# Kernel optimization log

Hardware: AMD Instinct MI355X
Metric: run time of the kernel (lower is better)

The kernel has to match this reference:

```python
import jax, jax.numpy as jnp
import numpy as np

NUM_JOINTS = 32
N_E = 1024
E_DIM = 128
BETA = 0.25
HID = 256
CHAINS = [[0,1,2,3,4,5],[0,6,7,8,9,10],[0,11,12,13,14,15],
          [12,16,17,18,19,20,21,22,23],[12,24,25,26,27,28,29,30,31]]


def setup_inputs() -> dict:
    key = jax.random.key(0)
    ks = jax.random.split(key, 8)
    B, T = 64, 128
    z = jax.random.normal(ks[0], (B, T, NUM_JOINTS, E_DIM), jnp.float32)
    # xavier_uniform for embeddings: bound = sqrt(6/(n_e+e_dim))
    eb = float(np.sqrt(6.0 / (N_E + E_DIM)))
    emb = jax.random.uniform(ks[1], (NUM_JOINTS, N_E, E_DIM), jnp.float32, -eb, eb)
    # torch Linear default init: U(-1/sqrt(fan_in), 1/sqrt(fan_in))
    b1b = float(1.0 / np.sqrt(2 * E_DIM))
    W1 = jax.random.uniform(ks[2], (2 * E_DIM, HID), jnp.float32, -b1b, b1b)
    b1 = jax.random.uniform(ks[3], (HID,), jnp.float32, -b1b, b1b)
    ln_g = jnp.ones((HID,), jnp.float32)
    ln_b = jnp.zeros((HID,), jnp.float32)
    b2b = float(1.0 / np.sqrt(HID))
    W2 = jax.random.uniform(ks[4], (HID, E_DIM), jnp.float32, -b2b, b2b)
    b2 = jax.random.uniform(ks[5], (E_DIM,), jnp.float32, -b2b, b2b)
    return {"z": z, "emb": emb, "W1": W1, "b1": b1, "ln_g": ln_g,
            "ln_b": ln_b, "W2": W2, "b2": b2}


def _layernorm(x, g, b, eps=1e-5):
    m = jnp.mean(x, axis=-1, keepdims=True)
    v = jnp.mean((x - m) ** 2, axis=-1, keepdims=True)
    return (x - m) * jax.lax.rsqrt(v + eps) * g + b


def _mlp(x, W1, b1, ln_g, ln_b, W2, b2):
    h = x @ W1 + b1
    h = jax.nn.relu(_layernorm(h, ln_g, ln_b))
    return h @ W2 + b2


def _quantize_joint(h, E):
    # h: [B,T,C], E: [n_e,C]. argmin of euclidean dist == argmin of -2 h.E^T + |E|^2
    B, T, C = h.shape
    hf = h.reshape(-1, C)
    d = -2.0 * (hf @ E.T) + jnp.sum(E * E, axis=1)  # [B*T, n_e]
    idx = jnp.argmin(d, axis=1)
    e = E[idx].reshape(B, T, C)  # one-hot @ E == gather
    sg = jax.lax.stop_gradient
    loss = jnp.mean((sg(e) - h) ** 2) + BETA * jnp.mean((e - sg(h)) ** 2)
    q = h + sg(e - h)  # straight-through
    return q, e, idx.reshape(B, T), loss


def reference(z, emb, W1, b1, ln_g, ln_b, W2, b2):
    B, T, V, C = z.shape
    sg = jax.lax.stop_gradient
    stored_q, stored_e, stored_idx = {}, {}, {}
    total = jnp.zeros((), z.dtype)
    for chain in CHAINS:
        parent_e = None
        for i, j in enumerate(chain):
            if j not in stored_q:  # single-pass per joint
                zj = z[:, :, j, :]
                h = _mlp(jnp.concatenate([parent_e, zj], -1), W1, b1, ln_g, ln_b, W2, b2) if i > 0 else zj
                q, e, idx, loss = _quantize_joint(h, emb[j])
                stored_q[j], stored_e[j], stored_idx[j] = q, e, idx
                total = total + loss
            parent_e = sg(stored_e[j])
    z_q = jnp.stack([stored_q[v] for v in range(V)], axis=2)      # [B,T,V,C]
    indices = jnp.stack([stored_idx[v] for v in range(V)], axis=2)  # [B,T,V]
    return z_q, total / V, indices
```

## Files before the change

kernel.cpp:

```cpp
#include <hip/hip_runtime.h>

#define NJ 32
#define NE 1024
#define CD 128
#define HID 256
#define ROWS 8192

struct Lv { int nj; int j[5]; int p[5]; };

__global__ __launch_bounds__(256) void norms_kernel(const float* __restrict__ emb,
                                                    float* __restrict__ nrm) {
  int gid = blockIdx.x * 256 + threadIdx.x;
  int n = gid >> 2, l = gid & 3;
  const float* row = emb + (size_t)n * CD;
  float s = 0.f;
#pragma unroll
  for (int i = 0; i < 8; ++i) {
    float4 v = *(const float4*)&row[(l + 4 * i) * 4];
    s += v.x * v.x + v.y * v.y + v.z * v.z + v.w * v.w;
  }
  s += __shfl_xor(s, 1);
  s += __shfl_xor(s, 2);
  if (l == 0) nrm[n] = s;
}

template <int RB>
__global__ __launch_bounds__(256) void fused_level(
    const float* __restrict__ z, const float* __restrict__ emb,
    const float* __restrict__ W1, const float* __restrict__ b1,
    const float* __restrict__ lng, const float* __restrict__ lnb,
    const float* __restrict__ W2, const float* __restrict__ b2,
    const float* __restrict__ nrm,
    float* __restrict__ zq, float* __restrict__ idx_out,
    float* __restrict__ partials, Lv lv, int pbase) {
  constexpr int RPG = RB / 8;
  constexpr int R4 = RB / 4;
  constexpr int HSP = RB + 4;
  constexpr int BPJ = ROWS / RB;
  constexpr int XS_SZ = 32 * HSP;
  constexpr int HS_SZ = 128 * HSP;
  constexpr int P1 = XS_SZ + 8448;
  constexpr int P3 = HS_SZ + 2112;
  constexpr int P4 = HS_SZ + 16 * 516 + 512;
  constexpr int SM12 = (P1 > P3) ? P1 : P3;
  constexpr int SMEM = (SM12 > P4) ? SM12 : P4;

  __shared__ __align__(16) float smem[SMEM];
  __shared__ float wsum[4];
  float* xs  = smem;
  float* ws1 = smem + XS_SZ;
  float* as_ = smem;
  float* ws2 = smem + HS_SZ;
  float* hs  = smem;
  float* es  = smem + HS_SZ;
  float* nsm = smem + HS_SZ + 16 * 516;

  const int tid = threadIdx.x;
  const int rg = tid >> 5, cg = tid & 31;
  const int u = cg & 15;
  const int qcA = (cg >> 4) * 128 + u * 4;
  const int qcB = qcA + 64;
  const int jl = blockIdx.x / BPJ;
  const int row0 = (blockIdx.x % BPJ) * RB;
  const int jj = lv.j[jl], pj = lv.p[jl];
  const size_t rstride = (size_t)NJ * CD;

  if (pj >= 0) {
    float acc1[RPG][8];
#pragma unroll
    for (int r = 0; r < RPG; ++r)
#pragma unroll
      for (int c = 0; c < 8; ++c) acc1[r][c] = 0.f;

#pragma unroll 1
    for (int ks = 0; ks < 8; ++ks) {
#pragma unroll
      for (int uu = 0; uu < RB / 32; ++uu) {
        int idx = uu * 256 + tid;
        int r = idx >> 3, kq = idx & 7;
        const float* src = (ks < 4)
            ? (zq + (size_t)(row0 + r) * rstride + (size_t)pj * CD + (ks * 32 + kq * 4))
            : (z  + (size_t)(row0 + r) * rstride + (size_t)jj * CD + (ks * 32 - 128 + kq * 4));
        float4 v = *(const float4*)src;
        xs[(kq * 4 + 0) * HSP + r] = v.x;
        xs[(kq * 4 + 1) * HSP + r] = v.y;
        xs[(kq * 4 + 2) * HSP + r] = v.z;
        xs[(kq * 4 + 3) * HSP + r] = v.w;
      }
#pragma unroll
      for (int v8 = 0; v8 < 8; ++v8) {
        int idx = v8 * 256 + tid;
        int k = idx >> 6, c4 = idx & 63;
        *(float4*)&ws1[k * 264 + c4 * 4] =
            *(const float4*)&W1[(size_t)(ks * 32 + k) * HID + c4 * 4];
      }
      __syncthreads();
#pragma unroll 2
      for (int kk = 0; kk < 32; ++kk) {
        float xr[RPG], wc[8];
#pragma unroll
        for (int g = 0; g < RPG / 4; ++g)
          *(float4*)&xr[g * 4] = *(const float4*)&xs[kk * HSP + rg * RPG + g * 4];
        *(float4*)&wc[0] = *(const float4*)&ws1[kk * 264 + qcA];
        *(float4*)&wc[4] = *(const float4*)&ws1[kk * 264 + qcB];
#pragma unroll
        for (int r = 0; r < RPG; ++r)
#pragma unroll
          for (int c = 0; c < 8; ++c)
            acc1[r][c] += xr[r] * wc[c];
      }
      __syncthreads();
    }

    {
      float bb[8], gg[8], be[8];
      *(float4*)&bb[0] = *(const float4*)&b1[qcA];
      *(float4*)&bb[4] = *(const float4*)&b1[qcB];
      *(float4*)&gg[0] = *(const float4*)&lng[qcA];
      *(float4*)&gg[4] = *(const float4*)&lng[qcB];
      *(float4*)&be[0] = *(const float4*)&lnb[qcA];
      *(float4*)&be[4] = *(const float4*)&lnb[qcB];
#pragma unroll
      for (int r = 0; r < RPG; ++r) {
        float s0 = 0.f, q0 = 0.f;
#pragma unroll
        for (int j = 0; j < 8; ++j) {
          float v = acc1[r][j] + bb[j];
          acc1[r][j] = v;
          s0 += v; q0 += v * v;
        }
        float si = __shfl_xor(s0, 16), qi = __shfl_xor(q0, 16);
        float s1 = si, q1 = qi;
#pragma unroll
        for (int j = 0; j < 8; ++j) {
          float v = acc1[r][j];
          s1 += v; q1 += v * v;
        }
#pragma unroll
        for (int m = 1; m < 16; m <<= 1) {
          s1 += __shfl_xor(s1, m); q1 += __shfl_xor(q1, m);
        }
        float s2 = __shfl_xor(s1, 16), q2 = __shfl_xor(q1, 16);
        float Sx = (cg & 16) ? s1 : s2;
        float Qx = (cg & 16) ? q1 : q2;
        float mu = Sx * (1.f / HID);
        float va = Qx * (1.f / HID) - mu * mu;
        float iv = 1.f / sqrtf(va + 1e-5f);
#pragma unroll
        for (int j = 0; j < 8; ++j) {
          float a = (acc1[r][j] - mu) * iv * gg[j] + be[j];
          acc1[r][j] = fmaxf(a, 0.f);
        }
      }
    }

    float acc2[RPG][4];
#pragma unroll
    for (int r = 0; r < RPG; ++r)
#pragma unroll
      for (int c = 0; c < 4; ++c) acc2[r][c] = 0.f;

#pragma unroll 1
    for (int half = 0; half < 2; ++half) {
      __syncthreads();
      if ((cg >> 4) == half) {
#pragma unroll
        for (int j = 0; j < 8; ++j) {
          int kl = (j >> 2) * 64 + u * 4 + (j & 3);
#pragma unroll
          for (int g = 0; g < RPG / 4; ++g)
            *(float4*)&as_[kl * HSP + rg * RPG + g * 4] =
                make_float4(acc1[g * 4 + 0][j], acc1[g * 4 + 1][j],
                            acc1[g * 4 + 2][j], acc1[g * 4 + 3][j]);
        }
      }
      __syncthreads();
#pragma unroll 1
      for (int kc = 0; kc < 8; ++kc) {
#pragma unroll
        for (int v = 0; v < 2; ++v) {
          int idx = v * 256 + tid;
          int k = idx >> 5, c4 = idx & 31;
          *(float4*)&ws2[k * 132 + c4 * 4] =
              *(const float4*)&W2[(size_t)(half * 128 + kc * 16 + k) * CD + c4 * 4];
        }
        __syncthreads();
#pragma unroll 2
        for (int kk = 0; kk < 16; ++kk) {
          float ar[RPG], wc2[4];
#pragma unroll
          for (int g = 0; g < RPG / 4; ++g)
            *(float4*)&ar[g * 4] =
                *(const float4*)&as_[(kc * 16 + kk) * HSP + rg * RPG + g * 4];
          *(float4*)&wc2[0] = *(const float4*)&ws2[kk * 132 + cg * 4];
#pragma unroll
          for (int r = 0; r < RPG; ++r)
#pragma unroll
            for (int c = 0; c < 4; ++c)
              acc2[r][c] += ar[r] * wc2[c];
        }
        __syncthreads();
      }
    }
    {
      float4 bv = *(const float4*)&b2[cg * 4];
      float bb2[4] = {bv.x, bv.y, bv.z, bv.w};
#pragma unroll
      for (int c = 0; c < 4; ++c) {
#pragma unroll
        for (int g = 0; g < RPG / 4; ++g)
          *(float4*)&hs[(cg * 4 + c) * HSP + rg * RPG + g * 4] =
              make_float4(acc2[g * 4 + 0][c] + bb2[c], acc2[g * 4 + 1][c] + bb2[c],
                          acc2[g * 4 + 2][c] + bb2[c], acc2[g * 4 + 3][c] + bb2[c]);
      }
    }
  } else {
#pragma unroll
    for (int v = 0; v < RB / 8; ++v) {
      int idx = v * 256 + tid;
      int r = idx >> 5, c4 = idx & 31;
      float4 vz = *(const float4*)&z[(size_t)(row0 + r) * rstride + (size_t)jj * CD + c4 * 4];
      hs[(c4 * 4 + 0) * HSP + r] = vz.x;
      hs[(c4 * 4 + 1) * HSP + r] = vz.y;
      hs[(c4 * 4 + 2) * HSP + r] = vz.z;
      hs[(c4 * 4 + 3) * HSP + r] = vz.w;
    }
  }

  const int w4 = tid >> 6;
  const int l4 = tid & 63;
  float mnv[R4]; int mni[R4];
#pragma unroll
  for (int r = 0; r < R4; ++r) { mnv[r] = 3.402823e38f; mni[r] = 0; }
  const float* embJ = emb + (size_t)jj * NE * CD;
  const float* nrmJ = nrm + jj * NE;

#pragma unroll 1
  for (int p = 0; p < 2; ++p) {
    __syncthreads();
    if (tid < 128) {
      *(float4*)&nsm[tid * 4] = *(const float4*)&nrmJ[p * 512 + tid * 4];
    }
    float acc4[R4][8];
#pragma unroll
    for (int r = 0; r < R4; ++r)
#pragma unroll
      for (int c = 0; c < 8; ++c) acc4[r][c] = 0.f;

#pragma unroll 1
    for (int kc = 0; kc < 8; ++kc) {
#pragma unroll
      for (int v = 0; v < 8; ++v) {
        int idx = v * 256 + tid;
        int n = idx >> 2, kq = idx & 3;
        float4 ev = *(const float4*)&embJ[(size_t)(p * 512 + n) * CD + kc * 16 + kq * 4];
        es[(kq * 4 + 0) * 516 + n] = ev.x;
        es[(kq * 4 + 1) * 516 + n] = ev.y;
        es[(kq * 4 + 2) * 516 + n] = ev.z;
        es[(kq * 4 + 3) * 516 + n] = ev.w;
      }
      __syncthreads();
#pragma unroll 2
      for (int kk = 0; kk < 16; ++kk) {
        int c = kc * 16 + kk;
        float hr[R4], ec[8];
#pragma unroll
        for (int g = 0; g < R4 / 4; ++g)
          *(float4*)&hr[g * 4] = *(const float4*)&hs[c * HSP + w4 * R4 + g * 4];
        *(float4*)&ec[0] = *(const float4*)&es[kk * 516 + l4 * 4];
        *(float4*)&ec[4] = *(const float4*)&es[kk * 516 + 256 + l4 * 4];
#pragma unroll
        for (int r = 0; r < R4; ++r)
#pragma unroll
          for (int c2 = 0; c2 < 8; ++c2)
            acc4[r][c2] += hr[r] * ec[c2];
      }
      __syncthreads();
    }
#pragma unroll
    for (int r = 0; r < R4; ++r) {
#pragma unroll
      for (int q = 0; q < 2; ++q) {
#pragma unroll
        for (int j = 0; j < 4; ++j) {
          int nl = q * 256 + l4 * 4 + j;
          float d = nsm[nl] - 2.f * acc4[r][q * 4 + j];
          int n = p * 512 + nl;
          if (d < mnv[r]) { mnv[r] = d; mni[r] = n; }
        }
      }
    }
  }

#pragma unroll
  for (int r = 0; r < R4; ++r) {
    float mv = mnv[r]; int mi = mni[r];
#pragma unroll
    for (int m = 1; m < 64; m <<= 1) {
      float om = __shfl_xor(mv, m); int oi = __shfl_xor(mi, m);
      if (om < mv || (om == mv && oi < mi)) { mv = om; mi = oi; }
    }
    mnv[r] = mv; mni[r] = mi;
  }

  float lsum = 0.f;
#pragma unroll
  for (int r = 0; r < R4; ++r) {
    int row = w4 * R4 + r;
    int id = mni[r];
    const float* erow = embJ + (size_t)id * CD;
    float2 ev = *(const float2*)&erow[l4 * 2];
    float h0 = hs[(l4 * 2 + 0) * HSP + row];
    float h1 = hs[(l4 * 2 + 1) * HSP + row];
    float dx = ev.x - h0, dy = ev.y - h1;
    lsum += dx * dx + dy * dy;
    *(float2*)&zq[(size_t)(row0 + row) * rstride + (size_t)jj * CD + l4 * 2] = ev;
    if (l4 == r) idx_out[(size_t)(row0 + row) * NJ + jj] = (float)id;
  }
#pragma unroll
  for (int m = 1; m < 64; m <<= 1) lsum += __shfl_xor(lsum, m);
  if (l4 == 0) wsum[w4] = lsum;
  __syncthreads();
  if (tid == 0) partials[pbase + blockIdx.x] = wsum[0] + wsum[1] + wsum[2] + wsum[3];
}

__global__ __launch_bounds__(256) void loss_reduce(const float* __restrict__ p, int n,
                                                   float* __restrict__ out) {
  __shared__ float ws[4];
  float s = 0.f;
  for (int i = threadIdx.x; i < n; i += 256) s += p[i];
#pragma unroll
  for (int m = 1; m < 64; m <<= 1) s += __shfl_xor(s, m);
  if ((threadIdx.x & 63) == 0) ws[threadIdx.x >> 6] = s;
  __syncthreads();
  if (threadIdx.x == 0)
    out[0] = (ws[0] + ws[1] + ws[2] + ws[3]) * (1.25f / (1048576.f * 32.f));
}

extern "C" void kernel_launch(void* const* d_in, const int* in_sizes, int n_in,
                              void* d_out, int out_size, void* d_ws, size_t ws_size,
                              hipStream_t stream) {
  const float* z = (const float*)d_in[0];
  const float* emb = (const float*)d_in[1];
  const float* W1 = (const float*)d_in[2];
  const float* b1 = (const float*)d_in[3];
  const float* lng = (const float*)d_in[4];
  const float* lnb = (const float*)d_in[5];
  const float* W2 = (const float*)d_in[6];
  const float* b2 = (const float*)d_in[7];

  float* zq = (float*)d_out;
  float* loss = zq + (size_t)ROWS * NJ * CD;
  float* idxo = loss + 1;

  float* nrm = (float*)d_ws;
  float* partials = nrm + NJ * NE;

  norms_kernel<<<NJ * NE * 4 / 256, 256, 0, stream>>>(emb, nrm);

  static const Lv levels[11] = {
      {1, {0, 0, 0, 0, 0}, {-1, 0, 0, 0, 0}},
      {3, {1, 6, 11, 0, 0}, {0, 0, 0, 0, 0}},
      {3, {2, 7, 12, 0, 0}, {1, 6, 11, 0, 0}},
      {5, {3, 8, 13, 16, 24}, {2, 7, 12, 12, 12}},
      {5, {4, 9, 14, 17, 25}, {3, 8, 13, 16, 24}},
      {5, {5, 10, 15, 18, 26}, {4, 9, 14, 17, 25}},
      {2, {19, 27, 0, 0, 0}, {18, 26, 0, 0, 0}},
      {2, {20, 28, 0, 0, 0}, {19, 27, 0, 0, 0}},
      {2, {21, 29, 0, 0, 0}, {20, 28, 0, 0, 0}},
      {2, {22, 30, 0, 0, 0}, {21, 29, 0, 0, 0}},
      {2, {23, 31, 0, 0, 0}, {22, 30, 0, 0, 0}},
  };
  static const int rbs[11] = {16, 64, 64, 64, 64, 64, 32, 32, 32, 32, 32};

  int pbase = 0;
  for (int L = 0; L < 11; ++L) {
    int bpj = ROWS / rbs[L];
    int blocks = levels[L].nj * bpj;
    if (rbs[L] == 64) {
      fused_level<64><<<blocks, 256, 0, stream>>>(
          z, emb, W1, b1, lng, lnb, W2, b2, nrm, zq, idxo, partials, levels[L], pbase);
    } else if (rbs[L] == 32) {
      fused_level<32><<<blocks, 256, 0, stream>>>(
          z, emb, W1, b1, lng, lnb, W2, b2, nrm, zq, idxo, partials, levels[L], pbase);
    } else {
      fused_level<16><<<blocks, 256, 0, stream>>>(
          z, emb, W1, b1, lng, lnb, W2, b2, nrm, zq, idxo, partials, levels[L], pbase);
    }
    pbase += blocks;
  }
  loss_reduce<<<1, 256, 0, stream>>>(partials, pbase, loss);
}
```

Measured before the change: 1.877 ms.

## Stage full MLP input once and read weights directly from global memory

The first MLP matmul now loads the whole 256-wide input tile into shared memory in one pass and runs a single K loop, reading W1 straight from global/L1 instead of staging 32-row chunks with per-chunk barriers. The second matmul is retiled to 16x16 threads with 8 output columns each, again reading W2 from global memory and removing its staged chunk loop. This is meant to cut barrier and shared-memory staging overhead. The cost is a larger input shared buffer, which may lower occupancy, and weight reads that now depend on cache hits.

Result: slower. 1.955 ms (+4.2%).

```diff
diff --git a/kernel.cpp b/kernel.cpp
--- a/kernel.cpp
+++ b/kernel.cpp
@@ -34,26 +34,22 @@
     float* __restrict__ zq, float* __restrict__ idx_out,
     float* __restrict__ partials, Lv lv, int pbase) {
   constexpr int RPG = RB / 8;
-  constexpr int R4 = RB / 4;
+  constexpr int R3  = RB / 16;
+  constexpr int R4  = RB / 4;
   constexpr int HSP = RB + 4;
   constexpr int BPJ = ROWS / RB;
-  constexpr int XS_SZ = 32 * HSP;
-  constexpr int HS_SZ = 128 * HSP;
-  constexpr int P1 = XS_SZ + 8448;
-  constexpr int P3 = HS_SZ + 2112;
-  constexpr int P4 = HS_SZ + 16 * 516 + 512;
-  constexpr int SM12 = (P1 > P3) ? P1 : P3;
-  constexpr int SMEM = (SM12 > P4) ? SM12 : P4;
+  constexpr int XS  = 256 * HSP;
+  constexpr int HS  = 128 * HSP;
+  constexpr int P4  = HS + 16 * 516 + 512;
+  constexpr int SMEM = (XS > P4) ? XS : P4;
 
   __shared__ __align__(16) float smem[SMEM];
   __shared__ float wsum[4];
   float* xs  = smem;
-  float* ws1 = smem + XS_SZ;
-  float* as_ = smem;
-  float* ws2 = smem + HS_SZ;
   float* hs  = smem;
-  float* es  = smem + HS_SZ;
-  float* nsm = smem + HS_SZ + 16 * 516;
+  float* as_ = smem + HS;
+  float* es  = smem + HS;
+  float* nsm = smem + HS + 16 * 516;
 
   const int tid = threadIdx.x;
   const int rg = tid >> 5, cg = tid & 31;
@@ -82,34 +78,31 @@
             ? (zq + (size_t)(row0 + r) * rstride + (size_t)pj * CD + (ks * 32 + kq * 4))
             : (z  + (size_t)(row0 + r) * rstride + (size_t)jj * CD + (ks * 32 - 128 + kq * 4));
         float4 v = *(const float4*)src;
-        xs[(kq * 4 + 0) * HSP + r] = v.x;
-        xs[(kq * 4 + 1) * HSP + r] = v.y;
-        xs[(kq * 4 + 2) * HSP + r] = v.z;
-        xs[(kq * 4 + 3) * HSP + r] = v.w;
-      }
-#pragma unroll
-      for (int v8 = 0; v8 < 8; ++v8) {
-        int idx = v8 * 256 + tid;
-        int k = idx >> 6, c4 = idx & 63;
-        *(float4*)&ws1[k * 264 + c4 * 4] =
-            *(const float4*)&W1[(size_t)(ks * 32 + k) * HID + c4 * 4];
-      }
-      __syncthreads();
-#pragma unroll 2
-      for (int kk = 0; kk < 32; ++kk) {
-        float xr[RPG], wc[8];
+        xs[(ks * 32 + kq * 4 + 0) * HSP + r] = v.x;
+        xs[(ks * 32 + kq * 4 + 1) * HSP + r] = v.y;
+        xs[(ks * 32 + kq * 4 + 2) * HSP + r] = v.z;
+        xs[(ks * 32 + kq * 4 + 3) * HSP + r] = v.w;
+      }
+    }
+    __syncthreads();
+#pragma unroll 4
+    for (int kk = 0; kk < 256; ++kk) {
+      float xr[RPG], wc[8];
+      if constexpr (RPG >= 4) {
 #pragma unroll
         for (int g = 0; g < RPG / 4; ++g)
           *(float4*)&xr[g * 4] = *(const float4*)&xs[kk * HSP + rg * RPG + g * 4];
-        *(float4*)&wc[0] = *(const float4*)&ws1[kk * 264 + qcA];
-        *(float4*)&wc[4] = *(const float4*)&ws1[kk * 264 + qcB];
-#pragma unroll
-        for (int r = 0; r < RPG; ++r)
-#pragma unroll
-          for (int c = 0; c < 8; ++c)
-            acc1[r][c] += xr[r] * wc[c];
-      }
-      __syncthreads();
+      } else {
+#pragma unroll
+        for (int g = 0; g < RPG; ++g) xr[g] = xs[kk * HSP + rg * RPG + g];
+      }
+      *(float4*)&wc[0] = *(const float4*)&W1[(size_t)kk * HID + qcA];
+      *(float4*)&wc[4] = *(const float4*)&W1[(size_t)kk * HID + qcB];
+#pragma unroll
+      for (int r = 0; r < RPG; ++r)
+#pragma unroll
+        for (int c = 0; c < 8; ++c)
+          acc1[r][c] += xr[r] * wc[c];
     }
 
     {
@@ -154,11 +147,13 @@
       }
     }
 
-    float acc2[RPG][4];
-#pragma unroll
-    for (int r = 0; r < RPG; ++r)
-#pragma unroll
-      for (int c = 0; c < 4; ++c) acc2[r][c] = 0.f;
+    const int cc = tid & 15, rr = tid >> 4;
+    const int qA = cc * 4, qB = qA + 64;
+    float acc2[R3][8];
+#pragma unroll
+    for (int r = 0; r < R3; ++r)
+#pragma unroll
+      for (int c = 0; c < 8; ++c) acc2[r][c] = 0.f;
 
 #pragma unroll 1
     for (int half = 0; half < 2; ++half) {
@@ -168,50 +163,42 @@
         for (int j = 0; j < 8; ++j) {
           int kl = (j >> 2) * 64 + u * 4 + (j & 3);
 #pragma unroll
-          for (int g = 0; g < RPG / 4; ++g)
-            *(float4*)&as_[kl * HSP + rg * RPG + g * 4] =
-                make_float4(acc1[g * 4 + 0][j], acc1[g * 4 + 1][j],
-                            acc1[g * 4 + 2][j], acc1[g * 4 + 3][j]);
+          for (int g = 0; g < RPG; ++g)
+            as_[kl * HSP + rg * RPG + g] = acc1[g][j];
         }
       }
       __syncthreads();
-#pragma unroll 1
-      for (int kc = 0; kc < 8; ++kc) {
-#pragma unroll
-        for (int v = 0; v < 2; ++v) {
-          int idx = v * 256 + tid;
-          int k = idx >> 5, c4 = idx & 31;
-          *(float4*)&ws2[k * 132 + c4 * 4] =
-              *(const float4*)&W2[(size_t)(half * 128 + kc * 16 + k) * CD + c4 * 4];
-        }
-        __syncthreads();
-#pragma unroll 2
-        for (int kk = 0; kk < 16; ++kk) {
-          float ar[RPG], wc2[4];
-#pragma unroll
-          for (int g = 0; g < RPG / 4; ++g)
-            *(float4*)&ar[g * 4] =
-                *(const float4*)&as_[(kc * 16 + kk) * HSP + rg * RPG + g * 4];
-          *(float4*)&wc2[0] = *(const float4*)&ws2[kk * 132 + cg * 4];
-#pragma unroll
-          for (int r = 0; r < RPG; ++r)
-#pragma unroll
-            for (int c = 0; c < 4; ++c)
-              acc2[r][c] += ar[r] * wc2[c];
-        }
-        __syncthreads();
+#pragma unroll 4
+      for (int kk = 0; kk < 128; ++kk) {
+        float ar[R3], wc2[8];
+        if constexpr (R3 >= 4) {
+#pragma unroll
+          for (int g = 0; g < R3 / 4; ++g)
+            *(float4*)&ar[g * 4] = *(const float4*)&as_[kk * HSP + rr * R3 + g * 4];
+        } else {
+#pragma unroll
+          for (int g = 0; g < R3; ++g) ar[g] = as_[kk * HSP + rr * R3 + g];
+        }
+        *(float4*)&wc2[0] = *(const float4*)&W2[(size_t)(half * 128 + kk) * CD + qA];
+        *(float4*)&wc2[4] = *(const float4*)&W2[(size_t)(half * 128 + kk) * CD + qB];
+#pragma unroll
+        for (int r = 0; r < R3; ++r)
+#pragma unroll
+          for (int c = 0; c < 8; ++c)
+            acc2[r][c] += ar[r] * wc2[c];
       }
     }
     {
-      float4 bv = *(const float4*)&b2[cg * 4];
-      float bb2[4] = {bv.x, bv.y, bv.z, bv.w};
-#pragma unroll
-      for (int c = 0; c < 4; ++c) {
-#pragma unroll
-        for (int g = 0; g < RPG / 4; ++g)
-          *(float4*)&hs[(cg * 4 + c) * HSP + rg * RPG + g * 4] =
-              make_float4(acc2[g * 4 + 0][c] + bb2[c], acc2[g * 4 + 1][c] + bb2[c],
-                          acc2[g * 4 + 2][c] + bb2[c], acc2[g * 4 + 3][c] + bb2[c]);
+      float bbA[4], bbB[4];
+      *(float4*)&bbA[0] = *(const float4*)&b2[qA];
+      *(float4*)&bbB[0] = *(const float4*)&b2[qB];
+#pragma unroll
+      for (int c = 0; c < 8; ++c) {
+        int col = (c < 4) ? (qA + c) : (qB + c - 4);
+        float bb2 = (c < 4) ? bbA[c] : bbB[c - 4];
+#pragma unroll
+        for (int r = 0; r < R3; ++r)
+          hs[col * HSP + rr * R3 + r] = acc2[r][c] + bb2;
       }
     }
   } else {
```
